# Kernel tuning notes

Hardware: AMD Instinct MI355X
Metric: run time of the kernel (lower is better)

## Reference

```python
import jax, jax.numpy as jnp
import numpy as np
from jax.ops import segment_sum, segment_max

N = 50000
E = 800000
F_IN = 128
F_HEAD = 32
HEADS = 8
N_CLASSES = 32
NEG_SLOPE = 0.2


def setup_inputs() -> dict:
    key = jax.random.key(0)
    ks = jax.random.split(key, 12)
    x = jax.random.normal(ks[0], (N, F_IN), dtype=jnp.float32)
    edge_index = jax.random.randint(ks[1], (2, E), 0, N, dtype=jnp.int64)
    # layer 1 params (in=128 -> heads=8, out=32)
    s1 = 1.0 / np.sqrt(F_IN)
    W1 = jax.random.uniform(ks[2], (F_IN, HEADS * F_HEAD), jnp.float32, -s1, s1)
    a_src1 = jax.random.uniform(ks[3], (HEADS, F_HEAD), jnp.float32, -s1, s1)
    a_dst1 = jax.random.uniform(ks[4], (HEADS, F_HEAD), jnp.float32, -s1, s1)
    b1 = jnp.zeros((HEADS * F_HEAD,), jnp.float32)
    # layer 2 params (in=256 -> heads=1, out=32)
    s2 = 1.0 / np.sqrt(HEADS * F_HEAD)
    W2 = jax.random.uniform(ks[5], (HEADS * F_HEAD, N_CLASSES), jnp.float32, -s2, s2)
    a_src2 = jax.random.uniform(ks[6], (1, N_CLASSES), jnp.float32, -s2, s2)
    a_dst2 = jax.random.uniform(ks[7], (1, N_CLASSES), jnp.float32, -s2, s2)
    b2 = jnp.zeros((N_CLASSES,), jnp.float32)
    return {"x": x, "edge_index": edge_index, "W1": W1, "a_src1": a_src1,
            "a_dst1": a_dst1, "b1": b1, "W2": W2, "a_src2": a_src2,
            "a_dst2": a_dst2, "b2": b2}


def gat_conv(x, W, a_src, a_dst, b, src, dst, heads, out_ch):
    n = x.shape[0]
    h = (x @ W).reshape(n, heads, out_ch)                  # [N,H,F]
    alpha_src = jnp.einsum('nhf,hf->nh', h, a_src)         # [N,H]
    alpha_dst = jnp.einsum('nhf,hf->nh', h, a_dst)
    e = alpha_src[src] + alpha_dst[dst]                    # [E,H]
    e = jnp.where(e > 0, e, NEG_SLOPE * e)                 # LeakyReLU(0.2)
    # segment softmax over edges grouped by destination node
    m = segment_max(e, dst, num_segments=n)                # [N,H]
    ex = jnp.exp(e - m[dst])
    denom = segment_sum(ex, dst, num_segments=n)           # [N,H]
    alpha = ex / (denom[dst] + 1e-16)                      # [E,H]
    out = segment_sum(alpha[:, :, None] * h[src], dst, num_segments=n)  # [N,H,F]
    return out.reshape(n, heads * out_ch) + b


def reference(x, edge_index, W1, a_src1, a_dst1, b1, W2, a_src2, a_dst2, b2):
    src, dst = edge_index[0], edge_index[1]
    h = gat_conv(x, W1, a_src1, a_dst1, b1, src, dst, HEADS, F_HEAD)
    h = jax.nn.elu(h)
    out = gat_conv(h, W2, a_src2, a_dst2, b2, src, dst, 1, N_CLASSES)
    return out
```

## Files before the change

### kernel.cpp

```cpp
#include <hip/hip_runtime.h>
#include <math.h>

#define NNODES 50000
#define NEDGES 800000
#define GB 782

typedef _Float16 f16;
typedef _Float16 f16x8 __attribute__((ext_vector_type(8)));
typedef _Float16 f16x4 __attribute__((ext_vector_type(4)));
typedef _Float16 f16x2 __attribute__((ext_vector_type(2)));
typedef float f32x4 __attribute__((ext_vector_type(4)));
typedef float f32x8 __attribute__((ext_vector_type(8)));
typedef unsigned short u16;


__global__ __launch_bounds__(256) void k_deg_wfrag(const int* __restrict__ ei, int* __restrict__ deg,
                                                   int* __restrict__ rank,
                                                   const float* __restrict__ W1, const float* __restrict__ W2,
                                                   f16* __restrict__ W1f, f16* __restrict__ W2f) {
    int bid = blockIdx.x;
    if (bid < NEDGES / 256) {
        int e = bid * 256 + threadIdx.x;
        rank[e] = atomicAdd(&deg[ei[NEDGES + e]], 1);
    } else {
        int id = (bid - NEDGES / 256) * 256 + threadIdx.x;
        if (id < 32768) {
            int k = id >> 8, c = id & 255;
            int kc = k >> 5, quad = (k & 31) >> 3, j = k & 7;
            W1f[(((kc << 8) + c) * 4 + quad) * 8 + j] = (f16)W1[id];
        } else {
            int i2 = id - 32768;
            int k = i2 >> 5, c = i2 & 31;
            int kc = k >> 5, quad = (k & 31) >> 3, j = k & 7;
            W2f[(((kc << 5) + c) * 4 + quad) * 8 + j] = (f16)W2[i2];
        }
    }
}

__global__ __launch_bounds__(256) void k_scanA(const int* __restrict__ deg, int* __restrict__ incl,
                                               int* __restrict__ partial) {
    int t = threadIdx.x;
    int i = blockIdx.x * 256 + t;
    int v = (i < NNODES) ? deg[i] : 0;
    int lane = t & 63, wid = t >> 6;
    int s = v;
#pragma unroll
    for (int d = 1; d < 64; d <<= 1) { int u = __shfl_up(s, d, 64); if (lane >= d) s += u; }
    __shared__ int wtot[4];
    if (lane == 63) wtot[wid] = s;
    __syncthreads();
    int off = 0;
    for (int w = 0; w < wid; ++w) off += wtot[w];
    s += off;
    if (i < NNODES) incl[i] = s;
    if (t == 255) partial[blockIdx.x] = s;
}

__global__ __launch_bounds__(256) void k_scanC(const int* __restrict__ deg, const int* __restrict__ incl,
                                               const int* __restrict__ partial, int* __restrict__ rowst) {
    int t = threadIdx.x, bid = blockIdx.x;
    int v = (t < bid) ? partial[t] : 0;
    int lane = t & 63, wid = t >> 6;
#pragma unroll
    for (int d = 1; d < 64; d <<= 1) v += __shfl_xor(v, d);
    __shared__ int ws[4];
    if (lane == 0) ws[wid] = v;
    __syncthreads();
    int choff = ws[0] + ws[1] + ws[2] + ws[3];
    int i = bid * 256 + t;
    if (i < NNODES) {
        int rs1 = incl[i] + choff;
        rowst[i + 1] = rs1;
        if (i == 0) rowst[0] = 0;
    }
}


__global__ __launch_bounds__(256) void k_gemm1_sc(const float* __restrict__ X, const f16* __restrict__ W1f,
                                                  const float* __restrict__ Asrc, const float* __restrict__ Adst,
                                                  f16* __restrict__ h1s, float* __restrict__ as1,
                                                  float* __restrict__ ad1, const int* __restrict__ ei,
                                                  const int* __restrict__ rowst, const int* __restrict__ rank,
                                                  u16* __restrict__ sd16) {
    __shared__ f16 sA[64 * 136];
    int bid = blockIdx.x;
    int t = threadIdx.x;
    if (bid >= GB) {
        int e = (bid - GB) * 256 + t;
        if (e < NEDGES) {
            int s = ei[e], d = ei[NEDGES + e];
            int pos = rowst[d] + rank[e];
            sd16[pos] = (u16)s;
        }
        return;
    }
    int bm = bid * 64;
    int lane = t & 63, w = t >> 6;
    int r = lane & 15, quad = lane >> 4;
    int cw = w * 64;
    f16x8 bf[4][4];
#pragma unroll
    for (int kc = 0; kc < 4; ++kc)
#pragma unroll
        for (int nt = 0; nt < 4; ++nt)
            bf[kc][nt] = *(const f16x8*)&W1f[(((kc << 8) + cw + nt * 16 + r) * 4 + quad) * 8];
#pragma unroll
    for (int i = 0; i < 8; ++i) {
        int idx = i * 256 + t;
        int row = idx >> 5, c4 = (idx & 31) << 2;
        int gr = bm + row;
        float4 v = make_float4(0.f, 0.f, 0.f, 0.f);
        if (gr < NNODES) v = *(const float4*)(X + (size_t)gr * 128 + c4);
        f16x4 h = {(f16)v.x, (f16)v.y, (f16)v.z, (f16)v.w};
        *(f16x4*)&sA[row * 136 + c4] = h;
    }
    __syncthreads();
    f32x4 acc[4][4];
#pragma unroll
    for (int rg = 0; rg < 4; ++rg)
#pragma unroll
        for (int nt = 0; nt < 4; ++nt) acc[rg][nt] = (f32x4){0.f, 0.f, 0.f, 0.f};
#pragma unroll
    for (int kc = 0; kc < 4; ++kc)
#pragma unroll
        for (int rg = 0; rg < 4; ++rg) {
            f16x8 a = *(f16x8*)&sA[(rg * 16 + r) * 136 + kc * 32 + quad * 8];
#pragma unroll
            for (int nt = 0; nt < 4; ++nt)
                acc[rg][nt] = __builtin_amdgcn_mfma_f32_16x16x32_f16(a, bf[kc][nt], acc[rg][nt], 0, 0, 0);
        }
#pragma unroll
    for (int rg = 0; rg < 4; ++rg)
#pragma unroll
        for (int nt = 0; nt < 4; ++nt)
#pragma unroll
            for (int i = 0; i < 4; ++i) {
                int gr = bm + rg * 16 + quad * 4 + i;
                if (gr < NNODES)
                    h1s[((size_t)(2 * w + (nt >> 1)) * NNODES + gr) * 32 + (nt & 1) * 16 + r] =
                        (f16)acc[rg][nt][i];
            }
    float asv[4], adv[4];
#pragma unroll
    for (int nt = 0; nt < 4; ++nt) {
        asv[nt] = Asrc[cw + nt * 16 + r];
        adv[nt] = Adst[cw + nt * 16 + r];
    }
#pragma unroll
    for (int rg = 0; rg < 4; ++rg)
#pragma unroll
        for (int i = 0; i < 4; ++i) {
            int gr = bm + rg * 16 + quad * 4 + i;
#pragma unroll
            for (int hh = 0; hh < 2; ++hh) {
                float ps = acc[rg][2 * hh][i] * asv[2 * hh] + acc[rg][2 * hh + 1][i] * asv[2 * hh + 1];
                float pd = acc[rg][2 * hh][i] * adv[2 * hh] + acc[rg][2 * hh + 1][i] * adv[2 * hh + 1];
#pragma unroll
                for (int off = 1; off < 16; off <<= 1) {
                    ps += __shfl_xor(ps, off);
                    pd += __shfl_xor(pd, off);
                }
                if (r == 0 && gr < NNODES) {
                    as1[(size_t)(2 * w + hh) * NNODES + gr] = ps;
                    ad1[(size_t)(2 * w + hh) * NNODES + gr] = pd;
                }
            }
        }
}

__global__ __launch_bounds__(256) void k_gemm2(const f16* __restrict__ h2s, const f16* __restrict__ W2f,
                                               const float* __restrict__ Asrc, const float* __restrict__ Adst,
                                               f16* __restrict__ gh, float* __restrict__ as2,
                                               float* __restrict__ ad2) {
    int t = threadIdx.x;
    int bm = blockIdx.x * 64;
    int lane = t & 63, w = t >> 6;
    int r = lane & 15, quad = lane >> 4;
    int r0 = w * 16;
    int gra = bm + r0 + r;
    int grac = gra < NNODES ? gra : 0;
    f32x4 acc[2];
    acc[0] = (f32x4){0.f, 0.f, 0.f, 0.f};
    acc[1] = (f32x4){0.f, 0.f, 0.f, 0.f};
#pragma unroll
    for (int kc = 0; kc < 8; ++kc) {
        f16x8 a = *(const f16x8*)(h2s + ((size_t)kc * NNODES + grac) * 32 + quad * 8);
#pragma unroll
        for (int nt = 0; nt < 2; ++nt) {
            f16x8 b = *(const f16x8*)&W2f[(((kc << 5) + nt * 16 + r) * 4 + quad) * 8];
            acc[nt] = __builtin_amdgcn_mfma_f32_16x16x32_f16(a, b, acc[nt], 0, 0, 0);
        }
    }
#pragma unroll
    for (int nt = 0; nt < 2; ++nt)
#pragma unroll
        for (int i = 0; i < 4; ++i) {
            int gr = bm + r0 + quad * 4 + i;
            if (gr < NNODES) gh[(size_t)gr * 32 + nt * 16 + r] = (f16)acc[nt][i];
        }
    float as0 = Asrc[r], as16 = Asrc[16 + r];
    float ad0 = Adst[r], ad16 = Adst[16 + r];
#pragma unroll
    for (int i = 0; i < 4; ++i) {
        int gr = bm + r0 + quad * 4 + i;
        float ps = acc[0][i] * as0 + acc[1][i] * as16;
        float pd = acc[0][i] * ad0 + acc[1][i] * ad16;
#pragma unroll
        for (int off = 1; off < 16; off <<= 1) {
            ps += __shfl_xor(ps, off);
            pd += __shfl_xor(pd, off);
        }
        if (r == 0 && gr < NNODES) { as2[gr] = ps; ad2[gr] = pd; }
    }
}

__global__ __launch_bounds__(256) void k_agg1(const int* __restrict__ rowst, const u16* __restrict__ sd16,
                                              const float* __restrict__ as1, const float* __restrict__ ad1,
                                              const f16* __restrict__ h1s, const float* __restrict__ b1,
                                              f16* __restrict__ h2s) {
    int bid = blockIdx.x;
    int sl = bid & 7;
    int ng = bid >> 3;
    int t = threadIdx.x;
    int w = t >> 6, lane = t & 63;
    int g = lane >> 2, cs = lane & 3;
    int c0 = cs << 3;
    int n = ng * 64 + w * 16 + g;
    if (n >= NNODES) return;
    int s = rowst[n], e = rowst[n + 1];
    float adn = ad1[(size_t)sl * NNODES + n];
    const f16* __restrict__ hp = h1s + (size_t)sl * NNODES * 32 + c0;
    const float* __restrict__ ap = as1 + (size_t)sl * NNODES;
    f32x8 acc = (f32x8){0.f, 0.f, 0.f, 0.f, 0.f, 0.f, 0.f, 0.f};
    float sum = 0.f;
    int j = s;
    for (; j + 3 < e; j += 4) {
        int s0 = (int)sd16[j], s1 = (int)sd16[j + 1];
        int s2 = (int)sd16[j + 2], s3 = (int)sd16[j + 3];
        float x0 = ap[s0] + adn, x1 = ap[s1] + adn;
        float x2 = ap[s2] + adn, x3 = ap[s3] + adn;
        f16x8 v0 = *(const f16x8*)(hp + (size_t)s0 * 32);
        f16x8 v1 = *(const f16x8*)(hp + (size_t)s1 * 32);
        f16x8 v2 = *(const f16x8*)(hp + (size_t)s2 * 32);
        f16x8 v3 = *(const f16x8*)(hp + (size_t)s3 * 32);
        x0 = fmaxf(x0, 0.2f * x0);
        x1 = fmaxf(x1, 0.2f * x1);
        x2 = fmaxf(x2, 0.2f * x2);
        x3 = fmaxf(x3, 0.2f * x3);
        float e0 = __expf(x0), e1 = __expf(x1), e2 = __expf(x2), e3 = __expf(x3);
        sum += (e0 + e1) + (e2 + e3);
#pragma unroll
        for (int k = 0; k < 8; ++k)
            acc[k] += e0 * (float)v0[k] + e1 * (float)v1[k] + e2 * (float)v2[k] + e3 * (float)v3[k];
    }
    for (; j < e; ++j) {
        int s0 = (int)sd16[j];
        float x0 = ap[s0] + adn;
        f16x8 v0 = *(const f16x8*)(hp + (size_t)s0 * 32);
        x0 = fmaxf(x0, 0.2f * x0);
        float e0 = __expf(x0);
        sum += e0;
#pragma unroll
        for (int k = 0; k < 8; ++k) acc[k] += e0 * (float)v0[k];
    }
    float inv = 1.f / (sum + 1e-16f);
    float4 b0 = *(const float4*)(b1 + sl * 32 + c0);
    float4 b4 = *(const float4*)(b1 + sl * 32 + c0 + 4);
    float o[8] = {acc[0] * inv + b0.x, acc[1] * inv + b0.y, acc[2] * inv + b0.z, acc[3] * inv + b0.w,
                  acc[4] * inv + b4.x, acc[5] * inv + b4.y, acc[6] * inv + b4.z, acc[7] * inv + b4.w};
    f16x8 oh;
#pragma unroll
    for (int k = 0; k < 8; ++k) {
        float v = o[k];
        v = v > 0.f ? v : __expf(v) - 1.f;
        oh[k] = (f16)v;
    }
    *(f16x8*)(h2s + ((size_t)sl * NNODES + n) * 32 + c0) = oh;
}

__global__ __launch_bounds__(256) void k_agg2(const int* __restrict__ rowst, const u16* __restrict__ sd16,
                                              const float* __restrict__ as2, const float* __restrict__ ad2,
                                              const f16* __restrict__ gh, const float* __restrict__ b2,
                                              float* __restrict__ out) {
    int w = threadIdx.x >> 6, lane = threadIdx.x & 63;
    int n = blockIdx.x * 4 + w;
    int s = rowst[n], e = rowst[n + 1];
    int slot = lane >> 4;
    int cp = lane & 15;
    float adn = ad2[n];
    const f16* __restrict__ gp = gh + 2 * cp;
    float a0 = 0.f, a1 = 0.f, sum = 0.f;
    int j = s + slot;
    for (; j + 12 < e; j += 16) {
        int si[4];
#pragma unroll
        for (int u = 0; u < 4; ++u) si[u] = (int)sd16[j + 4 * u];
        float xv[4];
#pragma unroll
        for (int u = 0; u < 4; ++u) xv[u] = as2[si[u]];
        f16x2 vv[4];
#pragma unroll
        for (int u = 0; u < 4; ++u) vv[u] = *(const f16x2*)(gp + (size_t)si[u] * 32);
#pragma unroll
        for (int u = 0; u < 4; ++u) {
            float x = xv[u] + adn;
            x = fmaxf(x, 0.2f * x);
            float ee = __expf(x);
            sum += ee;
            a0 += ee * (float)vv[u][0];
            a1 += ee * (float)vv[u][1];
        }
    }
    for (; j + 4 < e; j += 8) {
        int s0 = (int)sd16[j];
        int s1 = (int)sd16[j + 4];
        float x0 = as2[s0] + adn, x1 = as2[s1] + adn;
        f16x2 v0 = *(const f16x2*)(gp + (size_t)s0 * 32);
        f16x2 v1 = *(const f16x2*)(gp + (size_t)s1 * 32);
        x0 = fmaxf(x0, 0.2f * x0);
        x1 = fmaxf(x1, 0.2f * x1);
        float e0 = __expf(x0), e1 = __expf(x1);
        sum += e0 + e1;
        a0 += e0 * (float)v0[0] + e1 * (float)v1[0];
        a1 += e0 * (float)v0[1] + e1 * (float)v1[1];
    }
    for (; j < e; j += 4) {
        int s0 = (int)sd16[j];
        float x0 = as2[s0] + adn;
        f16x2 v0 = *(const f16x2*)(gp + (size_t)s0 * 32);
        x0 = fmaxf(x0, 0.2f * x0);
        float e0 = __expf(x0);
        sum += e0;
        a0 += e0 * (float)v0[0];
        a1 += e0 * (float)v0[1];
    }
#pragma unroll
    for (int d = 16; d < 64; d <<= 1) {
        sum += __shfl_xor(sum, d);
        a0 += __shfl_xor(a0, d);
        a1 += __shfl_xor(a1, d);
    }
    if (slot == 0) {
        float inv = 1.f / (sum + 1e-16f);
        float2 o;
        o.x = a0 * inv + b2[2 * cp];
        o.y = a1 * inv + b2[2 * cp + 1];
        *(float2*)(out + (size_t)n * 32 + 2 * cp) = o;
    }
}


extern "C" void kernel_launch(void* const* d_in, const int* in_sizes, int n_in,
                              void* d_out, int out_size, void* d_ws, size_t ws_size,
                              hipStream_t stream) {
    const float* x    = (const float*)d_in[0];
    const int*   ei   = (const int*)d_in[1];
    const float* W1   = (const float*)d_in[2];
    const float* As1  = (const float*)d_in[3];
    const float* Ad1  = (const float*)d_in[4];
    const float* b1   = (const float*)d_in[5];
    const float* W2   = (const float*)d_in[6];
    const float* As2  = (const float*)d_in[7];
    const float* Ad2  = (const float*)d_in[8];
    const float* b2   = (const float*)d_in[9];
    float* out = (float*)d_out;

    char* p = (char*)d_ws;
    auto alloc = [&](size_t bytes) -> char* {
        char* r = p;
        p += (bytes + 255) & ~(size_t)255;
        return r;
    };
    f16* h1s      = (f16*)alloc((size_t)NNODES * 256 * 2);
    f16* h2s      = (f16*)alloc((size_t)NNODES * 256 * 2);
    f16* W1f      = (f16*)alloc((size_t)128 * 256 * 2);
    f16* W2f      = (f16*)alloc((size_t)256 * 32 * 2);
    f16* gh       = (f16*)alloc((size_t)NNODES * 32 * 2);
    float* asrc1  = (float*)alloc((size_t)NNODES * 8 * 4);
    float* adst1  = (float*)alloc((size_t)NNODES * 8 * 4);
    float* asrc2  = (float*)alloc((size_t)NNODES * 4);
    float* adst2  = (float*)alloc((size_t)NNODES * 4);
    int* deg      = (int*)alloc((size_t)NNODES * 4);
    int* incl     = (int*)alloc((size_t)NNODES * 4);
    int* rowst    = (int*)alloc((size_t)(NNODES + 1) * 4);
    int* rank     = (int*)alloc((size_t)NEDGES * 4);
    u16* sdc      = (u16*)alloc((size_t)NEDGES * 2);
    int* partial  = (int*)alloc(256 * 4);

    const int EB = NEDGES / 256;
    const int NCH = (NNODES + 255) / 256;

    hipMemsetAsync(deg, 0, (size_t)NNODES * 4, stream);
    k_deg_wfrag<<<EB + 160, 256, 0, stream>>>(ei, deg, rank, W1, W2, W1f, W2f);
    k_scanA<<<NCH, 256, 0, stream>>>(deg, incl, partial);
    k_scanC<<<NCH, 256, 0, stream>>>(deg, incl, partial, rowst);

    k_gemm1_sc<<<GB + EB, 256, 0, stream>>>(x, W1f, As1, Ad1, h1s, asrc1, adst1, ei, rowst, rank, sdc);
    k_agg1<<<8 * GB, 256, 0, stream>>>(rowst, sdc, asrc1, adst1, h1s, b1, h2s);

    k_gemm2<<<(NNODES + 63) / 64, 256, 0, stream>>>(h2s, W2f, As2, Ad2, gh, asrc2, adst2);
    k_agg2<<<NNODES / 4, 256, 0, stream>>>(rowst, sdc, asrc2, adst2, gh, b2, out);
}
```

Before: 254.5 us.

## Sort nodes by in-degree for layer-1 aggregation and unroll edge loop by eight

Builds a degree histogram and its exclusive scan, then a counting-sort permutation of nodes by in-degree (capped at 511), computed in extra blocks of the GEMM/scatter kernel. The layer-1 aggregation processes nodes in that permuted order so the lanes of a wavefront handle nodes of similar degree, which cuts divergence from the variable-length edge loops. It also adds an 8-way unrolled edge loop that issues all index, score and feature gathers before the math, to raise memory-level parallelism. The cost is more atomics, an extra permutation read, scattered output writes, and higher register pressure.

```diff
diff --git a/kernel.cpp b/kernel.cpp
--- a/kernel.cpp
+++ b/kernel.cpp
@@ -4,6 +4,7 @@
 #define NNODES 50000
 #define NEDGES 800000
 #define GB 782
+#define PB 196
 
 typedef _Float16 f16;
 typedef _Float16 f16x8 __attribute__((ext_vector_type(8)));
@@ -38,10 +39,11 @@
 }
 
 __global__ __launch_bounds__(256) void k_scanA(const int* __restrict__ deg, int* __restrict__ incl,
-                                               int* __restrict__ partial) {
+                                               int* __restrict__ partial, int* __restrict__ hist) {
     int t = threadIdx.x;
     int i = blockIdx.x * 256 + t;
     int v = (i < NNODES) ? deg[i] : 0;
+    if (i < NNODES) atomicAdd(&hist[v < 511 ? v : 511], 1);
     int lane = t & 63, wid = t >> 6;
     int s = v;
 #pragma unroll
@@ -57,7 +59,8 @@
 }
 
 __global__ __launch_bounds__(256) void k_scanC(const int* __restrict__ deg, const int* __restrict__ incl,
-                                               const int* __restrict__ partial, int* __restrict__ rowst) {
+                                               const int* __restrict__ partial, int* __restrict__ rowst,
+                                               int* __restrict__ hist) {
     int t = threadIdx.x, bid = blockIdx.x;
     int v = (t < bid) ? partial[t] : 0;
     int lane = t & 63, wid = t >> 6;
@@ -73,6 +76,17 @@
         rowst[i + 1] = rs1;
         if (i == 0) rowst[0] = 0;
     }
+    if (bid == 0 && t < 64) {
+        int hv[8], loc = 0;
+#pragma unroll
+        for (int k = 0; k < 8; ++k) { hv[k] = hist[t * 8 + k]; loc += hv[k]; }
+        int incl8 = loc;
+#pragma unroll
+        for (int d = 1; d < 64; d <<= 1) { int u = __shfl_up(incl8, d, 64); if (t >= d) incl8 += u; }
+        int off = incl8 - loc;
+#pragma unroll
+        for (int k = 0; k < 8; ++k) { int x = hv[k]; hist[t * 8 + k] = off; off += x; }
+    }
 }
 
 
@@ -81,10 +95,21 @@
                                                   f16* __restrict__ h1s, float* __restrict__ as1,
                                                   float* __restrict__ ad1, const int* __restrict__ ei,
                                                   const int* __restrict__ rowst, const int* __restrict__ rank,
-                                                  u16* __restrict__ sd16) {
+                                                  u16* __restrict__ sd16, const int* __restrict__ deg,
+                                                  int* __restrict__ hist, int* __restrict__ perm) {
     __shared__ f16 sA[64 * 136];
     int bid = blockIdx.x;
     int t = threadIdx.x;
+    if (bid >= GB + NEDGES / 256) {
+        int i = (bid - GB - NEDGES / 256) * 256 + t;
+        if (i < NNODES) {
+            int d = deg[i];
+            if (d > 511) d = 511;
+            int pos = atomicAdd(&hist[d], 1);
+            perm[pos] = i;
+        }
+        return;
+    }
     if (bid >= GB) {
         int e = (bid - GB) * 256 + t;
         if (e < NEDGES) {
@@ -217,7 +242,7 @@
 __global__ __launch_bounds__(256) void k_agg1(const int* __restrict__ rowst, const u16* __restrict__ sd16,
                                               const float* __restrict__ as1, const float* __restrict__ ad1,
                                               const f16* __restrict__ h1s, const float* __restrict__ b1,
-                                              f16* __restrict__ h2s) {
+                                              f16* __restrict__ h2s, const int* __restrict__ perm) {
     int bid = blockIdx.x;
     int sl = bid & 7;
     int ng = bid >> 3;
@@ -227,31 +252,53 @@
     int c0 = cs << 3;
     int n = ng * 64 + w * 16 + g;
     if (n >= NNODES) return;
-    int s = rowst[n], e = rowst[n + 1];
-    float adn = ad1[(size_t)sl * NNODES + n];
+    int nid = perm[n];
+    int s = rowst[nid], e = rowst[nid + 1];
+    float adn = ad1[(size_t)sl * NNODES + nid];
     const f16* __restrict__ hp = h1s + (size_t)sl * NNODES * 32 + c0;
     const float* __restrict__ ap = as1 + (size_t)sl * NNODES;
     f32x8 acc = (f32x8){0.f, 0.f, 0.f, 0.f, 0.f, 0.f, 0.f, 0.f};
     float sum = 0.f;
     int j = s;
+    for (; j + 7 < e; j += 8) {
+        int si[8];
+#pragma unroll
+        for (int u = 0; u < 8; ++u) si[u] = (int)sd16[j + u];
+        float xv[8];
+#pragma unroll
+        for (int u = 0; u < 8; ++u) xv[u] = ap[si[u]];
+        f16x8 vv[8];
+#pragma unroll
+        for (int u = 0; u < 8; ++u) vv[u] = *(const f16x8*)(hp + (size_t)si[u] * 32);
+#pragma unroll
+        for (int u = 0; u < 8; ++u) {
+            float x = xv[u] + adn;
+            x = fmaxf(x, 0.2f * x);
+            float ee = __expf(x);
+            sum += ee;
+#pragma unroll
+            for (int k = 0; k < 8; ++k) acc[k] += ee * (float)vv[u][k];
+        }
+    }
     for (; j + 3 < e; j += 4) {
-        int s0 = (int)sd16[j], s1 = (int)sd16[j + 1];
-        int s2 = (int)sd16[j + 2], s3 = (int)sd16[j + 3];
-        float x0 = ap[s0] + adn, x1 = ap[s1] + adn;
-        float x2 = ap[s2] + adn, x3 = ap[s3] + adn;
-        f16x8 v0 = *(const f16x8*)(hp + (size_t)s0 * 32);
-        f16x8 v1 = *(const f16x8*)(hp + (size_t)s1 * 32);
-        f16x8 v2 = *(const f16x8*)(hp + (size_t)s2 * 32);
-        f16x8 v3 = *(const f16x8*)(hp + (size_t)s3 * 32);
-        x0 = fmaxf(x0, 0.2f * x0);
-        x1 = fmaxf(x1, 0.2f * x1);
-        x2 = fmaxf(x2, 0.2f * x2);
-        x3 = fmaxf(x3, 0.2f * x3);
-        float e0 = __expf(x0), e1 = __expf(x1), e2 = __expf(x2), e3 = __expf(x3);
-        sum += (e0 + e1) + (e2 + e3);
-#pragma unroll
-        for (int k = 0; k < 8; ++k)
-            acc[k] += e0 * (float)v0[k] + e1 * (float)v1[k] + e2 * (float)v2[k] + e3 * (float)v3[k];
+        int si[4];
+#pragma unroll
+        for (int u = 0; u < 4; ++u) si[u] = (int)sd16[j + u];
+        float xv[4];
+#pragma unroll
+        for (int u = 0; u < 4; ++u) xv[u] = ap[si[u]];
+        f16x8 vv[4];
+#pragma unroll
+        for (int u = 0; u < 4; ++u) vv[u] = *(const f16x8*)(hp + (size_t)si[u] * 32);
+#pragma unroll
+        for (int u = 0; u < 4; ++u) {
+            float x = xv[u] + adn;
+            x = fmaxf(x, 0.2f * x);
+            float ee = __expf(x);
+            sum += ee;
+#pragma unroll
+            for (int k = 0; k < 8; ++k) acc[k] += ee * (float)vv[u][k];
+        }
     }
     for (; j < e; ++j) {
         int s0 = (int)sd16[j];
@@ -275,7 +322,7 @@
         v = v > 0.f ? v : __expf(v) - 1.f;
         oh[k] = (f16)v;
     }
-    *(f16x8*)(h2s + ((size_t)sl * NNODES + n) * 32 + c0) = oh;
+    *(f16x8*)(h2s + ((size_t)sl * NNODES + nid) * 32 + c0) = oh;
 }
 
 __global__ __launch_bounds__(256) void k_agg2(const int* __restrict__ rowst, const u16* __restrict__ sd16,
@@ -386,17 +433,21 @@
     int* rank     = (int*)alloc((size_t)NEDGES * 4);
     u16* sdc      = (u16*)alloc((size_t)NEDGES * 2);
     int* partial  = (int*)alloc(256 * 4);
+    int* hist     = (int*)alloc(512 * 4);
+    int* perm     = (int*)alloc((size_t)NNODES * 4);
 
     const int EB = NEDGES / 256;
     const int NCH = (NNODES + 255) / 256;
 
     hipMemsetAsync(deg, 0, (size_t)NNODES * 4, stream);
+    hipMemsetAsync(hist, 0, 512 * 4, stream);
     k_deg_wfrag<<<EB + 160, 256, 0, stream>>>(ei, deg, rank, W1, W2, W1f, W2f);
-    k_scanA<<<NCH, 256, 0, stream>>>(deg, incl, partial);
-    k_scanC<<<NCH, 256, 0, stream>>>(deg, incl, partial, rowst);
-
-    k_gemm1_sc<<<GB + EB, 256, 0, stream>>>(x, W1f, As1, Ad1, h1s, asrc1, adst1, ei, rowst, rank, sdc);
-    k_agg1<<<8 * GB, 256, 0, stream>>>(rowst, sdc, asrc1, adst1, h1s, b1, h2s);
+    k_scanA<<<NCH, 256, 0, stream>>>(deg, incl, partial, hist);
+    k_scanC<<<NCH, 256, 0, stream>>>(deg, incl, partial, rowst, hist);
+
+    k_gemm1_sc<<<GB + EB + PB, 256, 0, stream>>>(x, W1f, As1, Ad1, h1s, asrc1, adst1, ei, rowst, rank,
+                                                 sdc, deg, hist, perm);
+    k_agg1<<<8 * GB, 256, 0, stream>>>(rowst, sdc, asrc1, adst1, h1s, b1, h2s, perm);
 
     k_gemm2<<<(NNODES + 63) / 64, 256, 0, stream>>>(h2s, W2f, As2, Ad2, gh, asrc2, adst2);
     k_agg2<<<NNODES / 4, 256, 0, stream>>>(rowst, sdc, asrc2, adst2, gh, b2, out);
```

Result: slower. 528.3 us (+107.6%).
